# Kernel optimization log

Hardware: AMD Instinct MI355X
Metric: run time of the kernel (lower is better)

Reference implementation:

```python
import jax, jax.numpy as jnp
import numpy as np

TRAIN_WAY = 5
TRAIN_SHOT = 5
N_LOCAL = 100  # == h*w, so Conv1d(kernel=stride=n_local) pools each class segment


def setup_inputs() -> dict:
    key = jax.random.key(0)
    k1, k2, k3 = jax.random.split(key, 3)
    t, wq, ws, c, h, w = 4, 75, 25, 640, 10, 10
    return {
        "query_feat": jax.random.normal(k1, (t, wq, c, h, w), dtype=jnp.float32),
        "support_feat": jax.random.normal(k2, (t, ws, c, h, w), dtype=jnp.float32),
        "conv_w": jax.random.normal(k3, (1, 1, N_LOCAL), dtype=jnp.float32) * 0.1,
        "conv_b": jnp.zeros((1,), dtype=jnp.float32),
    }


def reference(query_feat, support_feat, conv_w, conv_b):
    t, wq, c, h, w = query_feat.shape
    hw = h * w
    way, shot = TRAIN_WAY, TRAIN_SHOT

    # ---- support covariance per (t, way) ----
    s = support_feat.reshape(t, way * shot, c, hw).transpose(0, 1, 3, 2)  # (t, ws, hw, c)
    s = s.reshape(t, way, shot * hw, c)
    s = s - jnp.mean(s, axis=2, keepdims=True)
    cov = jnp.einsum('twnc,twnd->twcd', s, s) / (hw - 1)  # (t, way, c, c)

    # ---- query features centered over spatial positions ----
    q = query_feat.reshape(t, wq, c, hw).transpose(0, 1, 3, 2)  # (t, wq, hw, c)
    q = q - jnp.mean(q, axis=2, keepdims=True)

    # diag(Q @ Cov @ Q^T) == sum((Q @ Cov) * Q, -1)  -- same math, no hw x hw intermediate
    qc = jnp.einsum('tqnc,twcd->tqwnd', q, cov)          # (t, wq, way, hw, c)
    cov_sim = jnp.sum(qc * q[:, :, None], axis=-1)       # (t, wq, way, hw)

    # ---- LeakyReLU(0.2) -> Dropout (eval: identity) -> Conv1d(k=stride=hw) ----
    x = jnp.where(cov_sim >= 0, cov_sim, 0.2 * cov_sim)
    # conv with kernel=stride=hw over length way*hw == per-segment dot product
    score = jnp.einsum('tqwn,n->tqw', x, conv_w[0, 0]) + conv_b[0]
    return score  # (t, wq, way)
```

## Files before the change

### kernel.cpp

```cpp
#include <hip/hip_runtime.h>

#define T     4
#define WQ    75
#define C     640
#define HW    100
#define WAY   5
#define SHOT  5
#define NT    5
#define NPAIR 15

#define QOCT  14
#define QTS   (QOCT*128*8)
#define SOCT  64
#define STS   (SOCT*128*8)

#define WS_COVB_OFF  0
#define WS_QTB_OFF   9830400
#define WS_QTBW_OFF  52838400
#define WS_STB_OFF   95846400

typedef __attribute__((ext_vector_type(8)))  short bfrag8;
typedef __attribute__((ext_vector_type(16))) float f32x16;

__device__ __forceinline__ unsigned short f2bf(float x) {
    unsigned int u = __float_as_uint(x);
    return (unsigned short)((u + 0x7fffu + ((u >> 16) & 1u)) >> 16);
}
__device__ __forceinline__ float bflo(unsigned u) { return __uint_as_float(u << 16); }
__device__ __forceinline__ float bfhi(unsigned u) { return __uint_as_float(u & 0xffff0000u); }

__device__ __forceinline__ void pair_ij(int p, int& ti, int& tj) {
    int base = 0;
    #pragma unroll
    for (int a = 0; a < NT; ++a) {
        int cnt = NT - a;
        if (p < base + cnt) { ti = a; tj = a + (p - base); return; }
        base += cnt;
    }
    ti = 0; tj = 0;
}

#define LD2S 505
struct SpackSh { float ld2[16 * LD2S]; float mpart2[16][16]; float mean2[16]; };
struct QpackSh { float ld[32 * 101]; float wl[HW]; float mpart[32][4]; float mean[32]; };
union PackSh { SpackSh s; QpackSh q; };

__global__ __launch_bounds__(256, 4)
void pack_kernel(const float* __restrict__ qf, const float* __restrict__ sf,
                 const float* __restrict__ convw, const float* __restrict__ bias,
                 unsigned short* __restrict__ stb, unsigned short* __restrict__ qtb,
                 unsigned short* __restrict__ qtbw, float* __restrict__ out) {
    __shared__ PackSh sh;
    int bid = blockIdx.x, tid = threadIdx.x;

    if (bid < 800) {
        int rb = bid % 40, tw = bid / 40;
        int r0 = rb * 16;
        for (int sh_i = 0; sh_i < SHOT; ++sh_i) {
            const float* src = sf + ((size_t)(tw * SHOT + sh_i) * C + r0) * HW;
            #pragma unroll
            for (int it = 0; it < 2; ++it) {
                int idx = tid + it * 256;
                if (idx < 400) {
                    float4 v = ((const float4*)src)[idx];
                    int f = idx * 4;
                    int row = f / HW, n = f % HW;
                    float* d = &sh.s.ld2[row * LD2S + sh_i * HW + n];
                    d[0] = v.x; d[1] = v.y; d[2] = v.z; d[3] = v.w;
                }
            }
        }
        __syncthreads();
        {
            int row = tid & 15, part = tid >> 4;
            float ps = 0.f;
            #pragma unroll
            for (int i = 0; i < 32; ++i) {
                int k = part * 32 + i;
                if (k < 500) ps += sh.s.ld2[row * LD2S + k];
            }
            sh.s.mpart2[row][part] = ps;
        }
        __syncthreads();
        if (tid < 16) {
            float s2 = 0.f;
            #pragma unroll
            for (int p2 = 0; p2 < 16; ++p2) s2 += sh.s.mpart2[tid][p2];
            sh.s.mean2[tid] = s2 * (1.0f / (SHOT * HW));
        }
        __syncthreads();
        #pragma unroll
        for (int it = 0; it < 4; ++it) {
            int task = tid + it * 256;
            int row = task & 15, oct = task >> 4;
            float m = sh.s.mean2[row];
            unsigned short ob[8] __attribute__((aligned(16)));
            #pragma unroll
            for (int j = 0; j < 8; ++j) {
                int k = oct * 8 + j;
                ob[j] = (k < 500) ? f2bf(sh.s.ld2[row * LD2S + k] - m) : (unsigned short)0;
            }
            int crow = r0 + row;
            int tile = crow >> 7, trow = crow & 127;
            size_t dst = ((((size_t)tw * NT + tile) * SOCT + oct) * 128 + trow) * 8;
            *(uint4*)(stb + dst) = *(uint4*)ob;
        }
    } else {
        int idx0 = bid - 800;
        int cb = idx0 % 20, tq = idx0 / 20;
        if (idx0 == 0) {
            float b = bias[0];
            for (int i = tid; i < T * WQ * WAY; i += 256) out[i] = b;
        }
        if (tid < HW) sh.q.wl[tid] = convw[tid];
        const float* src = qf + ((size_t)tq * C + cb * 32) * HW;
        #pragma unroll
        for (int it = 0; it < 4; ++it) {
            int idx = tid + it * 256;
            if (idx < 800) {
                float4 v = ((const float4*)src)[idx];
                int f = idx * 4;
                int row = f / HW, n = f % HW;
                float* d = &sh.q.ld[row * 101 + n];
                d[0] = v.x; d[1] = v.y; d[2] = v.z; d[3] = v.w;
            }
        }
        __syncthreads();
        if (tid < 128) {
            int row = tid & 31, part = tid >> 5;
            float ps = 0.f;
            #pragma unroll
            for (int i = 0; i < 25; ++i) ps += sh.q.ld[row * 101 + part * 25 + i];
            sh.q.mpart[row][part] = ps;
        }
        __syncthreads();
        if (tid < 32) sh.q.mean[tid] = (sh.q.mpart[tid][0] + sh.q.mpart[tid][1]
                                      + sh.q.mpart[tid][2] + sh.q.mpart[tid][3]) * (1.0f / HW);
        __syncthreads();
        int crow0 = cb * 32;
        int tile = crow0 >> 7, trowbase = crow0 & 127;
        #pragma unroll
        for (int it = 0; it < 2; ++it) {
            int task = tid + it * 256;
            if (task < 32 * QOCT) {
                int row = task & 31, oct = task >> 5;
                float m = sh.q.mean[row];
                unsigned short ob[8] __attribute__((aligned(16)));
                unsigned short ow[8] __attribute__((aligned(16)));
                #pragma unroll
                for (int j = 0; j < 8; ++j) {
                    int n = oct * 8 + j;
                    float v = (n < HW) ? (sh.q.ld[row * 101 + n] - m) : 0.f;
                    float w = (n < HW) ? sh.q.wl[n] : 0.f;
                    ob[j] = f2bf(v); ow[j] = f2bf(v * w);
                }
                size_t dst = ((((size_t)tq * NT + tile) * QOCT + oct) * 128 + trowbase + row) * 8;
                *(uint4*)(qtb + dst)  = *(uint4*)ob;
                *(uint4*)(qtbw + dst) = *(uint4*)ow;
            }
        }
    }
}

__global__ __launch_bounds__(256, 3)
void cov_kernel(const unsigned short* __restrict__ stb, unsigned short* __restrict__ covb) {
    int bid = blockIdx.x, tid = threadIdx.x;
    int p = bid % NPAIR, tw = bid / NPAIR;
    int ti, tj; pair_ij(p, ti, tj);
    int lane = tid & 63, wave = tid >> 6;
    int qm = wave & 1, qn = wave >> 1, lh = lane >> 5, ls = lane & 31;
    int rA = qm * 64 + ls, rB = qn * 64 + ls;
    const unsigned short* Ab = stb + ((size_t)tw * NT + ti) * STS;
    const unsigned short* Bb = stb + ((size_t)tw * NT + tj) * STS;

    f32x16 acc[4];
    #pragma unroll
    for (int b = 0; b < 4; ++b)
        #pragma unroll
        for (int e = 0; e < 16; ++e) acc[b][e] = 0.f;

    #pragma unroll 4
    for (int s = 0; s < 32; ++s) {
        int oc = s * 2 + lh;
        const unsigned short* ap = Ab + (size_t)oc * 1024;
        const unsigned short* bp = Bb + (size_t)oc * 1024;
        bfrag8 a0 = *(const bfrag8*)&ap[rA * 8];
        bfrag8 a1 = *(const bfrag8*)&ap[(rA + 32) * 8];
        bfrag8 b0 = *(const bfrag8*)&bp[rB * 8];
        bfrag8 b1 = *(const bfrag8*)&bp[(rB + 32) * 8];
        acc[0] = __builtin_amdgcn_mfma_f32_32x32x16_bf16(a0, b0, acc[0], 0, 0, 0);
        acc[1] = __builtin_amdgcn_mfma_f32_32x32x16_bf16(a0, b1, acc[1], 0, 0, 0);
        acc[2] = __builtin_amdgcn_mfma_f32_32x32x16_bf16(a1, b0, acc[2], 0, 0, 0);
        acc[3] = __builtin_amdgcn_mfma_f32_32x32x16_bf16(a1, b1, acc[3], 0, 0, 0);
    }

    const float inv = 1.0f / (HW - 1);
    unsigned short* cbp = covb + ((size_t)tw * NPAIR + p) * 16384;
    #pragma unroll
    for (int b = 0; b < 4; ++b) {
        unsigned ow[8];
        #pragma unroll
        for (int wd = 0; wd < 8; ++wd)
            ow[wd] = (unsigned)f2bf(acc[b][2 * wd] * inv)
                   | ((unsigned)f2bf(acc[b][2 * wd + 1] * inv) << 16);
        size_t off = (size_t)((wave * 4 + b) * 64 + lane) * 16;
        *(uint4*)(cbp + off)     = *(uint4*)&ow[0];
        *(uint4*)(cbp + off + 8) = *(uint4*)&ow[4];
    }
}

__global__ __launch_bounds__(256, 3)
void score_kernel(const unsigned short* __restrict__ qtb, const unsigned short* __restrict__ qtbw,
                  const unsigned short* __restrict__ covb, float* __restrict__ out) {
    __shared__ float red[4][WAY];
    int orig = blockIdx.x;
    int xcd = orig & 7, slot = orig >> 3;
    int wgid = (xcd < 4) ? (xcd * 563 + slot) : (2252 + (xcd - 4) * 562 + slot);
    int p = wgid % NPAIR;
    int tq = wgid / NPAIR;
    int t = tq / WQ, q = tq % WQ;
    int ti, tj; pair_ij(p, ti, tj);
    int tid = threadIdx.x, lane = tid & 63, wave = tid >> 6;
    int qm = wave & 1, qn = wave >> 1, lh = lane >> 5, ls = lane & 31;
    int rA = qm * 64 + ls, rB = qn * 64 + ls;
    float mult = (ti == tj) ? 1.0f : 2.0f;

    const unsigned short* Ab = qtbw + ((size_t)(t * WQ + q) * NT + ti) * QTS;
    const unsigned short* Bb = qtb  + ((size_t)(t * WQ + q) * NT + tj) * QTS;

    f32x16 acc[4];
    #pragma unroll
    for (int b = 0; b < 4; ++b)
        #pragma unroll
        for (int e = 0; e < 16; ++e) acc[b][e] = 0.f;

    #pragma unroll
    for (int s = 0; s < 7; ++s) {
        int oc = s * 2 + lh;
        const unsigned short* ap = Ab + (size_t)oc * 1024;
        const unsigned short* bp = Bb + (size_t)oc * 1024;
        bfrag8 a0 = *(const bfrag8*)&ap[rA * 8];
        bfrag8 a1 = *(const bfrag8*)&ap[(rA + 32) * 8];
        bfrag8 b0 = *(const bfrag8*)&bp[rB * 8];
        bfrag8 b1 = *(const bfrag8*)&bp[(rB + 32) * 8];
        acc[0] = __builtin_amdgcn_mfma_f32_32x32x16_bf16(a0, b0, acc[0], 0, 0, 0);
        acc[1] = __builtin_amdgcn_mfma_f32_32x32x16_bf16(a0, b1, acc[1], 0, 0, 0);
        acc[2] = __builtin_amdgcn_mfma_f32_32x32x16_bf16(a1, b0, acc[2], 0, 0, 0);
        acc[3] = __builtin_amdgcn_mfma_f32_32x32x16_bf16(a1, b1, acc[3], 0, 0, 0);
    }

    const unsigned short* cb0 = covb + ((size_t)(t * WAY) * NPAIR + p) * 16384
                              + (size_t)(wave * 4096 + lane * 16);
    #pragma unroll 1
    for (int w = 0; w < WAY; ++w) {
        const unsigned short* cbw = cb0 + (size_t)w * (NPAIR * 16384);
        uint4 cu[8];
        #pragma unroll
        for (int b = 0; b < 4; ++b) {
            cu[2 * b]     = *(const uint4*)(cbw + b * 1024);
            cu[2 * b + 1] = *(const uint4*)(cbw + b * 1024 + 8);
        }
        float s0 = 0.f, s1 = 0.f, s2 = 0.f, s3 = 0.f;
        #pragma unroll
        for (int b = 0; b < 4; ++b) {
            #pragma unroll
            for (int h = 0; h < 2; ++h) {
                uint4 u = cu[2 * b + h];
                int e = h * 8;
                s0 += bflo(u.x) * acc[b][e + 0] + bfhi(u.x) * acc[b][e + 1];
                s1 += bflo(u.y) * acc[b][e + 2] + bfhi(u.y) * acc[b][e + 3];
                s2 += bflo(u.z) * acc[b][e + 4] + bfhi(u.z) * acc[b][e + 5];
                s3 += bflo(u.w) * acc[b][e + 6] + bfhi(u.w) * acc[b][e + 7];
            }
        }
        float v = ((s0 + s1) + (s2 + s3)) * mult;
        #pragma unroll
        for (int off2 = 32; off2 > 0; off2 >>= 1) v += __shfl_down(v, off2);
        if (lane == 0) red[wave][w] = v;
    }
    __syncthreads();
    if (tid < WAY) {
        float tot = red[0][tid] + red[1][tid] + red[2][tid] + red[3][tid];
        atomicAdd(&out[(size_t)(t * WQ + q) * WAY + tid], tot);
    }
}

extern "C" void kernel_launch(void* const* d_in, const int* in_sizes, int n_in,
                              void* d_out, int out_size, void* d_ws, size_t ws_size,
                              hipStream_t stream) {
    const float* qf = (const float*)d_in[0];
    const float* sf = (const float*)d_in[1];
    const float* cw = (const float*)d_in[2];
    const float* cb = (const float*)d_in[3];
    float* out = (float*)d_out;

    unsigned short* covb = (unsigned short*)((char*)d_ws + WS_COVB_OFF);
    unsigned short* qtb  = (unsigned short*)((char*)d_ws + WS_QTB_OFF);
    unsigned short* qtbw = (unsigned short*)((char*)d_ws + WS_QTBW_OFF);
    unsigned short* stb  = (unsigned short*)((char*)d_ws + WS_STB_OFF);

    pack_kernel<<<6800, 256, 0, stream>>>(qf, sf, cw, cb, stb, qtb, qtbw, out);
    cov_kernel<<<300, 256, 0, stream>>>(stb, covb);
    score_kernel<<<4500, 256, 0, stream>>>(qtb, qtbw, covb, out);
}
```

Baseline: 222.0 us.

## Double-buffer covariance loads in score kernel and halve support pack rows

The score kernel now issues the first covariance tile load before the MFMA loop and double-buffers the remaining way tiles, so global loads overlap the Frobenius dot products; launch bounds drop to 2 blocks per CU to make room for the extra registers. The support pack path processes 8 channel rows per block instead of 16, doubling its block count and raising pack occupancy to 8. The aim is to hide covariance load latency and spread pack work more widely, at the cost of lower score-kernel occupancy from higher register pressure.

```diff
diff --git a/kernel.cpp b/kernel.cpp
--- a/kernel.cpp
+++ b/kernel.cpp
@@ -41,11 +41,13 @@
 }
 
 #define LD2S 505
-struct SpackSh { float ld2[16 * LD2S]; float mpart2[16][16]; float mean2[16]; };
+#define SROWS 8
+#define NSPACK (20 * (C / SROWS))
+struct SpackSh { float ld2[SROWS * LD2S]; float mpart2[SROWS][32]; float mean2[SROWS]; };
 struct QpackSh { float ld[32 * 101]; float wl[HW]; float mpart[32][4]; float mean[32]; };
 union PackSh { SpackSh s; QpackSh q; };
 
-__global__ __launch_bounds__(256, 4)
+__global__ __launch_bounds__(256, 8)
 void pack_kernel(const float* __restrict__ qf, const float* __restrict__ sf,
                  const float* __restrict__ convw, const float* __restrict__ bias,
                  unsigned short* __restrict__ stb, unsigned short* __restrict__ qtb,
@@ -53,46 +55,42 @@
     __shared__ PackSh sh;
     int bid = blockIdx.x, tid = threadIdx.x;
 
-    if (bid < 800) {
-        int rb = bid % 40, tw = bid / 40;
-        int r0 = rb * 16;
+    if (bid < NSPACK) {
+        int rb = bid % 80, tw = bid / 80;
+        int r0 = rb * SROWS;
         for (int sh_i = 0; sh_i < SHOT; ++sh_i) {
             const float* src = sf + ((size_t)(tw * SHOT + sh_i) * C + r0) * HW;
-            #pragma unroll
-            for (int it = 0; it < 2; ++it) {
-                int idx = tid + it * 256;
-                if (idx < 400) {
-                    float4 v = ((const float4*)src)[idx];
-                    int f = idx * 4;
-                    int row = f / HW, n = f % HW;
-                    float* d = &sh.s.ld2[row * LD2S + sh_i * HW + n];
-                    d[0] = v.x; d[1] = v.y; d[2] = v.z; d[3] = v.w;
-                }
+            if (tid < 200) {
+                float4 v = ((const float4*)src)[tid];
+                int f = tid * 4;
+                int row = f / HW, n = f % HW;
+                float* d = &sh.s.ld2[row * LD2S + sh_i * HW + n];
+                d[0] = v.x; d[1] = v.y; d[2] = v.z; d[3] = v.w;
             }
         }
         __syncthreads();
         {
-            int row = tid & 15, part = tid >> 4;
+            int row = tid & 7, part = tid >> 3;
             float ps = 0.f;
             #pragma unroll
-            for (int i = 0; i < 32; ++i) {
-                int k = part * 32 + i;
+            for (int i = 0; i < 16; ++i) {
+                int k = part * 16 + i;
                 if (k < 500) ps += sh.s.ld2[row * LD2S + k];
             }
             sh.s.mpart2[row][part] = ps;
         }
         __syncthreads();
-        if (tid < 16) {
+        if (tid < SROWS) {
             float s2 = 0.f;
             #pragma unroll
-            for (int p2 = 0; p2 < 16; ++p2) s2 += sh.s.mpart2[tid][p2];
+            for (int p2 = 0; p2 < 32; ++p2) s2 += sh.s.mpart2[tid][p2];
             sh.s.mean2[tid] = s2 * (1.0f / (SHOT * HW));
         }
         __syncthreads();
         #pragma unroll
-        for (int it = 0; it < 4; ++it) {
+        for (int it = 0; it < 2; ++it) {
             int task = tid + it * 256;
-            int row = task & 15, oct = task >> 4;
+            int row = task & 7, oct = task >> 3;
             float m = sh.s.mean2[row];
             unsigned short ob[8] __attribute__((aligned(16)));
             #pragma unroll
@@ -106,7 +104,7 @@
             *(uint4*)(stb + dst) = *(uint4*)ob;
         }
     } else {
-        int idx0 = bid - 800;
+        int idx0 = bid - NSPACK;
         int cb = idx0 % 20, tq = idx0 / 20;
         if (idx0 == 0) {
             float b = bias[0];
@@ -209,7 +207,27 @@
     }
 }
 
-__global__ __launch_bounds__(256, 3)
+#define CSTEP (NPAIR * 16384)
+#define LOADW(dst, src) { \
+    _Pragma("unroll") \
+    for (int b = 0; b < 4; ++b) { \
+        dst[2*b]   = *(const uint4*)((src) + b * 1024); \
+        dst[2*b+1] = *(const uint4*)((src) + b * 1024 + 8); } }
+#define FROB(buf, sout) { \
+    float s0 = 0.f, s1 = 0.f, s2 = 0.f, s3 = 0.f; \
+    _Pragma("unroll") \
+    for (int b = 0; b < 4; ++b) { \
+        _Pragma("unroll") \
+        for (int h = 0; h < 2; ++h) { \
+            uint4 u = buf[2*b + h]; \
+            int e = h * 8; \
+            s0 += bflo(u.x) * acc[b][e + 0] + bfhi(u.x) * acc[b][e + 1]; \
+            s1 += bflo(u.y) * acc[b][e + 2] + bfhi(u.y) * acc[b][e + 3]; \
+            s2 += bflo(u.z) * acc[b][e + 4] + bfhi(u.z) * acc[b][e + 5]; \
+            s3 += bflo(u.w) * acc[b][e + 6] + bfhi(u.w) * acc[b][e + 7]; } } \
+    sout = (s0 + s1) + (s2 + s3); }
+
+__global__ __launch_bounds__(256, 2)
 void score_kernel(const unsigned short* __restrict__ qtb, const unsigned short* __restrict__ qtbw,
                   const unsigned short* __restrict__ covb, float* __restrict__ out) {
     __shared__ float red[4][WAY];
@@ -227,6 +245,11 @@
 
     const unsigned short* Ab = qtbw + ((size_t)(t * WQ + q) * NT + ti) * QTS;
     const unsigned short* Bb = qtb  + ((size_t)(t * WQ + q) * NT + tj) * QTS;
+    const unsigned short* cb0 = covb + ((size_t)(t * WAY) * NPAIR + p) * 16384
+                              + (size_t)(wave * 4096 + lane * 16);
+
+    uint4 cuA[8], cuB[8];
+    LOADW(cuA, cb0)
 
     f32x16 acc[4];
     #pragma unroll
@@ -249,31 +272,20 @@
         acc[3] = __builtin_amdgcn_mfma_f32_32x32x16_bf16(a1, b1, acc[3], 0, 0, 0);
     }
 
-    const unsigned short* cb0 = covb + ((size_t)(t * WAY) * NPAIR + p) * 16384
-                              + (size_t)(wave * 4096 + lane * 16);
-    #pragma unroll 1
+    float sw[WAY];
+    LOADW(cuB, cb0 + 1 * CSTEP)
+    FROB(cuA, sw[0])
+    LOADW(cuA, cb0 + 2 * CSTEP)
+    FROB(cuB, sw[1])
+    LOADW(cuB, cb0 + 3 * CSTEP)
+    FROB(cuA, sw[2])
+    LOADW(cuA, cb0 + 4 * CSTEP)
+    FROB(cuB, sw[3])
+    FROB(cuA, sw[4])
+
+    #pragma unroll
     for (int w = 0; w < WAY; ++w) {
-        const unsigned short* cbw = cb0 + (size_t)w * (NPAIR * 16384);
-        uint4 cu[8];
-        #pragma unroll
-        for (int b = 0; b < 4; ++b) {
-            cu[2 * b]     = *(const uint4*)(cbw + b * 1024);
-            cu[2 * b + 1] = *(const uint4*)(cbw + b * 1024 + 8);
-        }
-        float s0 = 0.f, s1 = 0.f, s2 = 0.f, s3 = 0.f;
-        #pragma unroll
-        for (int b = 0; b < 4; ++b) {
-            #pragma unroll
-            for (int h = 0; h < 2; ++h) {
-                uint4 u = cu[2 * b + h];
-                int e = h * 8;
-                s0 += bflo(u.x) * acc[b][e + 0] + bfhi(u.x) * acc[b][e + 1];
-                s1 += bflo(u.y) * acc[b][e + 2] + bfhi(u.y) * acc[b][e + 3];
-                s2 += bflo(u.z) * acc[b][e + 4] + bfhi(u.z) * acc[b][e + 5];
-                s3 += bflo(u.w) * acc[b][e + 6] + bfhi(u.w) * acc[b][e + 7];
-            }
-        }
-        float v = ((s0 + s1) + (s2 + s3)) * mult;
+        float v = sw[w] * mult;
         #pragma unroll
         for (int off2 = 32; off2 > 0; off2 >>= 1) v += __shfl_down(v, off2);
         if (lane == 0) red[wave][w] = v;
@@ -299,7 +311,7 @@
     unsigned short* qtbw = (unsigned short*)((char*)d_ws + WS_QTBW_OFF);
     unsigned short* stb  = (unsigned short*)((char*)d_ws + WS_STB_OFF);
 
-    pack_kernel<<<6800, 256, 0, stream>>>(qf, sf, cw, cb, stb, qtb, qtbw, out);
+    pack_kernel<<<NSPACK + 6000, 256, 0, stream>>>(qf, sf, cw, cb, stb, qtb, qtbw, out);
     cov_kernel<<<300, 256, 0, stream>>>(stb, covb);
     score_kernel<<<4500, 256, 0, stream>>>(qtb, qtbw, covb, out);
 }
```

Measured after the change: 220.5 us. No clear change (-0.7%).
